# Performance work log

Measured on AMD Instinct MI355X. Metric: run time of the kernel, lower is better.

## Reference

```python
import jax, jax.numpy as jnp
import numpy as np
from jax import lax

SEQ_LEN, BC, NODES, FEAT, HID, NUM_LAYER = 12, 16, 1024, 32, 64, 2
NEG_BIG = -1e16


def _gru_layer(x_seq, w_ih, w_hh, b_ih, b_hh):
    # x_seq: [T, B, in]; PyTorch gate order r, z, n
    B = x_seq.shape[1]
    h0 = jnp.zeros((B, w_hh.shape[1]), dtype=x_seq.dtype)

    def step(h, x):
        gi = x @ w_ih.T + b_ih
        gh = h @ w_hh.T + b_hh
        ir, iz, inn = jnp.split(gi, 3, axis=-1)
        hr, hz, hn = jnp.split(gh, 3, axis=-1)
        r = jax.nn.sigmoid(ir + hr)
        zg = jax.nn.sigmoid(iz + hz)
        n = jnp.tanh(inn + r * hn)
        h_new = (1.0 - zg) * n + zg * h
        return h_new, h_new

    h_T, ys = lax.scan(step, h0, x_seq)
    return ys, h_T


def _gat_aggregate(z_, maskf):
    # z_: [bc, nodes, H]; inner-product attention with leaky_relu(0.1) and adjacency mask
    att = jnp.einsum('bnd,bmd->bnm', z_, z_)
    att = jax.nn.leaky_relu(att, negative_slope=0.1) * maskf[None]
    att = jnp.where(att == 0.0, NEG_BIG, att)  # masked_fill_(atten==0, -1e16)
    att = jax.nn.softmax(att, axis=2)
    return jnp.einsum('bnm,bmd->bnd', att, z_)


def setup_inputs() -> dict:
    key = jax.random.key(0)
    ks = jax.random.split(key, 12)
    s = 1.0 / np.sqrt(HID)
    inp = {
        'h': jax.random.normal(ks[0], (SEQ_LEN, BC, NODES, FEAT), dtype=jnp.float32),
        'mask': jax.random.randint(ks[1], (NODES, NODES), 0, 2, dtype=jnp.int32),
        'w_ih0': jax.random.uniform(ks[2], (3 * HID, FEAT), minval=-s, maxval=s),
        'w_hh0': jax.random.uniform(ks[3], (3 * HID, HID), minval=-s, maxval=s),
        'b_ih0': jax.random.uniform(ks[4], (3 * HID,), minval=-s, maxval=s),
        'b_hh0': jax.random.uniform(ks[5], (3 * HID,), minval=-s, maxval=s),
        'w_ih1': jax.random.uniform(ks[6], (3 * HID, HID), minval=-s, maxval=s),
        'w_hh1': jax.random.uniform(ks[7], (3 * HID, HID), minval=-s, maxval=s),
        'b_ih1': jax.random.uniform(ks[8], (3 * HID,), minval=-s, maxval=s),
        'b_hh1': jax.random.uniform(ks[9], (3 * HID,), minval=-s, maxval=s),
    }
    return inp


def reference(h, mask, w_ih0, w_hh0, b_ih0, b_hh0, w_ih1, w_hh1, b_ih1, b_hh1):
    x = h.reshape(SEQ_LEN, BC * NODES, FEAT)
    ys0, hT0 = _gru_layer(x, w_ih0, w_hh0, b_ih0, b_hh0)
    _, hT1 = _gru_layer(ys0, w_ih1, w_hh1, b_ih1, b_hh1)
    # z: [num_layer, bc, nodes, H]
    z = jnp.stack([hT0, hT1]).reshape(NUM_LAYER, BC, NODES, HID)
    maskf = mask.astype(z.dtype)
    h_agg = jax.vmap(_gat_aggregate, in_axes=(0, None))(z, maskf)
    return h_agg  # [num_layer, bc, nodes, H]
```

## Files before the change

### kernel.cpp

```cpp
#include <hip/hip_runtime.h>
#include <math.h>

#define SEQ 12
#define NBATCH 16384
#define FEAT 32
#define HID 64
#define NSPLIT 2

#define WP_IH0 0
#define WP_HH0 6144
#define WP_IH1 18432
#define WP_HH1 30720
#define WP_TOTAL 43008

typedef __attribute__((ext_vector_type(8))) short bf16x8;
typedef __attribute__((ext_vector_type(4))) float f32x4;

#define MFMA_B16(A,B,C) __builtin_amdgcn_mfma_f32_16x16x32_bf16((A),(B),(C),0,0,0)

union B8u { unsigned short s[8]; bf16x8 v; };

__device__ __forceinline__ float sigf(float x) { return 1.0f / (1.0f + __expf(-x)); }
__device__ __forceinline__ float tanh_fast(float x) { return 2.0f / (1.0f + __expf(-2.0f * x)) - 1.0f; }

__device__ __forceinline__ unsigned int packsplit(float v) {
  unsigned int u  = __float_as_uint(v);
  unsigned int hi = u & 0xFFFF0000u;
  unsigned int lo = __float_as_uint(v - __uint_as_float(hi)) >> 16;
  return hi | lo;
}

__device__ __forceinline__ void unpack8(const unsigned int* p, bf16x8& H, bf16x8& L) {
  uint4 u0 = *(const uint4*)p;
  uint4 u1 = *(const uint4*)(p + 4);
  unsigned int uu[8] = {u0.x, u0.y, u0.z, u0.w, u1.x, u1.y, u1.z, u1.w};
  B8u hh, ll;
  #pragma unroll
  for (int i = 0; i < 8; i++) {
    hh.s[i] = (unsigned short)(uu[i] >> 16);
    ll.s[i] = (unsigned short)(uu[i] & 0xFFFFu);
  }
  H = hh.v; L = ll.v;
}

__device__ __forceinline__ void split8(const float* fa, bf16x8& H, bf16x8& L) {
  B8u hh, ll;
  #pragma unroll
  for (int i = 0; i < 8; i++) {
    unsigned int u  = __float_as_uint(fa[i]);
    unsigned int hi = u & 0xFFFF0000u;
    hh.s[i] = (unsigned short)(hi >> 16);
    ll.s[i] = (unsigned short)(__float_as_uint(fa[i] - __uint_as_float(hi)) >> 16);
  }
  H = hh.v; L = ll.v;
}

#define DOT4(acc, A_, B_)                                   \
  acc = fmaf((A_).x, (B_).x, acc);                          \
  acc = fmaf((A_).y, (B_).y, acc);                          \
  acc = fmaf((A_).z, (B_).z, acc);                          \
  acc = fmaf((A_).w, (B_).w, acc);

__global__ void prep_frag_kernel(const float* __restrict__ w_ih0, const float* __restrict__ w_hh0,
                                 const float* __restrict__ w_ih1, const float* __restrict__ w_hh1,
                                 unsigned short* __restrict__ wf)
{
  int i = blockIdx.x * blockDim.x + threadIdx.x;
  if (i >= 43008) return;
  const float* src; int K, rel, baseS;
  if (i < 6144)       { src = w_ih0; K = 32; rel = i;         baseS = 0; }
  else if (i < 18432) { src = w_hh0; K = 64; rel = i - 6144;  baseS = 12288; }
  else if (i < 30720) { src = w_ih1; K = 64; rel = i - 18432; baseS = 36864; }
  else                { src = w_hh1; K = 64; rel = i - 30720; baseS = 61440; }
  int nks = K / 32;
  int fp   = rel >> 9;
  int lane = (rel >> 3) & 63;
  int e    = rel & 7;
  int ct = fp / nks, ks = fp % nks;
  int g = ct * 16 + (lane & 15);
  int k = ks * 32 + (lane >> 4) * 8 + e;
  float v = src[g * K + k];
  unsigned int u = __float_as_uint(v);
  unsigned short hi = (unsigned short)(u >> 16);
  float hif = __uint_as_float(u & 0xFFFF0000u);
  unsigned short lo = (unsigned short)(__float_as_uint(v - hif) >> 16);
  int out = baseS + fp * 1024 + lane * 8 + e;
  wf[out]       = hi;
  wf[out + 512] = lo;
}

__global__ void mask_pack(const int* __restrict__ mask, unsigned int* __restrict__ mbits)
{
  int i = blockIdx.x * blockDim.x + threadIdx.x;
  if (i >= 32768) return;
  int r = i >> 5, wd = i & 31;
  const int* mp = mask + (size_t)r * 1024 + wd * 32;
  unsigned int b = 0;
  #pragma unroll
  for (int k = 0; k < 32; k++) b |= (mp[k] != 0 ? 1u : 0u) << k;
  mbits[i] = b;
}

#define HSTR 72
__global__ __launch_bounds__(256, 2) void gru_fused(
    const float* __restrict__ x, const unsigned short* __restrict__ wf,
    const float* __restrict__ b_ih0, const float* __restrict__ b_hh0,
    const float* __restrict__ b_ih1, const float* __restrict__ b_hh1,
    unsigned int* __restrict__ zpk0, unsigned int* __restrict__ zpk1)
{
  __shared__ unsigned short h0h[2][16 * HSTR], h0o[2][16 * HSTR];
  __shared__ unsigned short h1h[2][16 * HSTR], h1o[2][16 * HSTR];
  const int tid = threadIdx.x;
  const int w = tid >> 6, l = tid & 63, lr = l & 15, lg = l >> 4;
  const int s0 = blockIdx.x * 16;
  const int j = w * 16 + lr;

  bf16x8 Wih0[3][2], Whh0[3][2][2], Wih1[3][2][2], Whh1[3][2][2];
  #pragma unroll
  for (int g = 0; g < 3; g++) {
    const int ct = w + g * 4;
    Wih0[g][0] = *(const bf16x8*)&wf[ct * 1024 + l * 8];
    Wih0[g][1] = *(const bf16x8*)&wf[ct * 1024 + 512 + l * 8];
    #pragma unroll
    for (int ks = 0; ks < 2; ks++) {
      Whh0[g][ks][0] = *(const bf16x8*)&wf[12288 + (ct * 2 + ks) * 1024 + l * 8];
      Whh0[g][ks][1] = *(const bf16x8*)&wf[12288 + (ct * 2 + ks) * 1024 + 512 + l * 8];
      Wih1[g][ks][0] = *(const bf16x8*)&wf[36864 + (ct * 2 + ks) * 1024 + l * 8];
      Wih1[g][ks][1] = *(const bf16x8*)&wf[36864 + (ct * 2 + ks) * 1024 + 512 + l * 8];
      Whh1[g][ks][0] = *(const bf16x8*)&wf[61440 + (ct * 2 + ks) * 1024 + l * 8];
      Whh1[g][ks][1] = *(const bf16x8*)&wf[61440 + (ct * 2 + ks) * 1024 + 512 + l * 8];
    }
  }

  const float br0  = b_ih0[j]      + b_hh0[j];
  const float bz0  = b_ih0[64 + j] + b_hh0[64 + j];
  const float bni0 = b_ih0[128 + j];
  const float bnh0 = b_hh0[128 + j];
  const float br1  = b_ih1[j]      + b_hh1[j];
  const float bz1  = b_ih1[64 + j] + b_hh1[64 + j];
  const float bni1 = b_ih1[128 + j];
  const float bnh1 = b_hh1[128 + j];

  for (int i = tid; i < 16 * HSTR; i += 256) {
    h0h[0][i] = 0; h0o[0][i] = 0; h1h[0][i] = 0; h1o[0][i] = 0;
  }
  float hD0[4] = {0.f, 0.f, 0.f, 0.f};
  float hD1[4] = {0.f, 0.f, 0.f, 0.f};
  __syncthreads();

  float4 xc0 = *(const float4*)(x + ((size_t)s0 + lr) * FEAT + lg * 8);
  float4 xc1 = *(const float4*)(x + ((size_t)s0 + lr) * FEAT + lg * 8 + 4);

  int pb = 0;
  #pragma unroll 1
  for (int t = 0; t < SEQ; t++) {
    const int cb = pb ^ 1;
    float4 xn0, xn1;
    if (t < SEQ - 1) {
      const float* xp = x + ((size_t)(t + 1) * NBATCH + s0 + lr) * FEAT + lg * 8;
      xn0 = *(const float4*)xp;
      xn1 = *(const float4*)(xp + 4);
    }

    f32x4 aR, aZ, aNI, aNH;
    #pragma unroll
    for (int e = 0; e < 4; e++) { aR[e] = br0; aZ[e] = bz0; aNI[e] = bni0; aNH[e] = bnh0; }
    {
      float fa[8] = {xc0.x, xc0.y, xc0.z, xc0.w, xc1.x, xc1.y, xc1.z, xc1.w};
      bf16x8 Ah, Al;
      split8(fa, Ah, Al);
      aR  = MFMA_B16(Ah, Wih0[0][0], aR);  aR  = MFMA_B16(Al, Wih0[0][0], aR);  aR  = MFMA_B16(Ah, Wih0[0][1], aR);
      aZ  = MFMA_B16(Ah, Wih0[1][0], aZ);  aZ  = MFMA_B16(Al, Wih0[1][0], aZ);  aZ  = MFMA_B16(Ah, Wih0[1][1], aZ);
      aNI = MFMA_B16(Ah, Wih0[2][0], aNI); aNI = MFMA_B16(Al, Wih0[2][0], aNI); aNI = MFMA_B16(Ah, Wih0[2][1], aNI);
    }
    #pragma unroll
    for (int ks = 0; ks < 2; ks++) {
      bf16x8 Ah = *(const bf16x8*)&h0h[pb][lr * HSTR + ks * 32 + lg * 8];
      bf16x8 Al = *(const bf16x8*)&h0o[pb][lr * HSTR + ks * 32 + lg * 8];
      aR  = MFMA_B16(Ah, Whh0[0][ks][0], aR);  aR  = MFMA_B16(Al, Whh0[0][ks][0], aR);  aR  = MFMA_B16(Ah, Whh0[0][ks][1], aR);
      aZ  = MFMA_B16(Ah, Whh0[1][ks][0], aZ);  aZ  = MFMA_B16(Al, Whh0[1][ks][0], aZ);  aZ  = MFMA_B16(Ah, Whh0[1][ks][1], aZ);
      aNH = MFMA_B16(Ah, Whh0[2][ks][0], aNH); aNH = MFMA_B16(Al, Whh0[2][ks][0], aNH); aNH = MFMA_B16(Ah, Whh0[2][ks][1], aNH);
    }
    #pragma unroll
    for (int e = 0; e < 4; e++) {
      float rg = sigf(aR[e]);
      float zg = sigf(aZ[e]);
      float n  = tanh_fast(fmaf(rg, aNH[e], aNI[e]));
      float hn = fmaf(zg, hD0[e] - n, n);
      hD0[e] = hn;
      unsigned int pk = packsplit(hn);
      int idx = (lg * 4 + e) * HSTR + j;
      h0h[cb][idx] = (unsigned short)(pk >> 16);
      h0o[cb][idx] = (unsigned short)(pk & 0xFFFFu);
    }
    __syncthreads();

    #pragma unroll
    for (int e = 0; e < 4; e++) { aR[e] = br1; aZ[e] = bz1; aNI[e] = bni1; aNH[e] = bnh1; }
    #pragma unroll
    for (int ks = 0; ks < 2; ks++) {
      bf16x8 Ah = *(const bf16x8*)&h0h[cb][lr * HSTR + ks * 32 + lg * 8];
      bf16x8 Al = *(const bf16x8*)&h0o[cb][lr * HSTR + ks * 32 + lg * 8];
      aR  = MFMA_B16(Ah, Wih1[0][ks][0], aR);  aR  = MFMA_B16(Al, Wih1[0][ks][0], aR);  aR  = MFMA_B16(Ah, Wih1[0][ks][1], aR);
      aZ  = MFMA_B16(Ah, Wih1[1][ks][0], aZ);  aZ  = MFMA_B16(Al, Wih1[1][ks][0], aZ);  aZ  = MFMA_B16(Ah, Wih1[1][ks][1], aZ);
      aNI = MFMA_B16(Ah, Wih1[2][ks][0], aNI); aNI = MFMA_B16(Al, Wih1[2][ks][0], aNI); aNI = MFMA_B16(Ah, Wih1[2][ks][1], aNI);
    }
    #pragma unroll
    for (int ks = 0; ks < 2; ks++) {
      bf16x8 Ah = *(const bf16x8*)&h1h[pb][lr * HSTR + ks * 32 + lg * 8];
      bf16x8 Al = *(const bf16x8*)&h1o[pb][lr * HSTR + ks * 32 + lg * 8];
      aR  = MFMA_B16(Ah, Whh1[0][ks][0], aR);  aR  = MFMA_B16(Al, Whh1[0][ks][0], aR);  aR  = MFMA_B16(Ah, Whh1[0][ks][1], aR);
      aZ  = MFMA_B16(Ah, Whh1[1][ks][0], aZ);  aZ  = MFMA_B16(Al, Whh1[1][ks][0], aZ);  aZ  = MFMA_B16(Ah, Whh1[1][ks][1], aZ);
      aNH = MFMA_B16(Ah, Whh1[2][ks][0], aNH); aNH = MFMA_B16(Al, Whh1[2][ks][0], aNH); aNH = MFMA_B16(Ah, Whh1[2][ks][1], aNH);
    }
    #pragma unroll
    for (int e = 0; e < 4; e++) {
      float rg = sigf(aR[e]);
      float zg = sigf(aZ[e]);
      float n  = tanh_fast(fmaf(rg, aNH[e], aNI[e]));
      float hn = fmaf(zg, hD1[e] - n, n);
      hD1[e] = hn;
      unsigned int pk = packsplit(hn);
      int idx = (lg * 4 + e) * HSTR + j;
      h1h[cb][idx] = (unsigned short)(pk >> 16);
      h1o[cb][idx] = (unsigned short)(pk & 0xFFFFu);
    }
    xc0 = xn0; xc1 = xn1;
    pb = cb;
  }

  #pragma unroll
  for (int e = 0; e < 4; e++) {
    int sl = lg * 4 + e;
    zpk0[(size_t)(s0 + sl) * 64 + j] = packsplit(hD0[e]);
    zpk1[(size_t)(s0 + sl) * 64 + j] = packsplit(hD1[e]);
  }
}

__global__ void prep_kernel(const float* __restrict__ w_ih0, const float* __restrict__ w_hh0,
                            const float* __restrict__ w_ih1, const float* __restrict__ w_hh1,
                            float* __restrict__ wp)
{
  for (int i = blockIdx.x * blockDim.x + threadIdx.x; i < WP_TOTAL; i += gridDim.x * blockDim.x) {
    const float* src;
    int K, rel;
    if (i < WP_HH0)      { src = w_ih0; K = 32; rel = i; }
    else if (i < WP_IH1) { src = w_hh0; K = 64; rel = i - WP_HH0; }
    else if (i < WP_HH1) { src = w_ih1; K = 64; rel = i - WP_IH1; }
    else                 { src = w_hh1; K = 64; rel = i - WP_HH1; }
    int kr = rel & 3;
    int jj = (rel >> 2) & 63;
    int rest = rel >> 8;
    int g = rest % 3;
    int k4 = rest / 3;
    wp[i] = src[(g * 64 + jj) * K + k4 * 4 + kr];
  }
}

__global__ __launch_bounds__(256, 1) void gru_fallback(
    const float* __restrict__ x, const float* __restrict__ wpack,
    const float* __restrict__ b_ih0, const float* __restrict__ b_hh0,
    const float* __restrict__ b_ih1, const float* __restrict__ b_hh1,
    unsigned int* __restrict__ zout)
{
  __shared__ float wlds[36864];
  __shared__ float h0s[16][64];
  __shared__ float h1s[16][64];
  const int tid = threadIdx.x;
  {
    const float4* src = (const float4*)(wpack + WP_HH0);
    float4* dst = (float4*)wlds;
    #pragma unroll 4
    for (int i = tid; i < 9216; i += 256) dst[i] = src[i];
  }
  const int j  = tid & 63;
  const int sg = __builtin_amdgcn_readfirstlane(tid >> 6);
  const float br0  = b_ih0[j]      + b_hh0[j];
  const float bz0  = b_ih0[64 + j] + b_hh0[64 + j];
  const float bni0 = b_ih0[128 + j];
  const float bnh0 = b_hh0[128 + j];
  const float br1  = b_ih1[j]      + b_hh1[j];
  const float bz1  = b_ih1[64 + j] + b_hh1[64 + j];
  const float bni1 = b_ih1[128 + j];
  const float bnh1 = b_hh1[128 + j];
  const int s0 = blockIdx.x * 16;
  float h0r[4] = {0.f, 0.f, 0.f, 0.f};
  float h1r[4] = {0.f, 0.f, 0.f, 0.f};
  #pragma unroll
  for (int ss = 0; ss < 4; ss++) { h0s[sg * 4 + ss][j] = 0.f; h1s[sg * 4 + ss][j] = 0.f; }
  __syncthreads();
  const float4* wih0g = (const float4*)(wpack + WP_IH0);
  const float4* whh0l = (const float4*)(wlds);
  const float4* wih1l = (const float4*)(wlds + 12288);
  const float4* whh1l = (const float4*)(wlds + 24576);
  for (int t = 0; t < SEQ; t++) {
    float ar[4], az[4], ani[4], anh[4];
    #pragma unroll
    for (int ss = 0; ss < 4; ss++) { ar[ss] = br0; az[ss] = bz0; ani[ss] = bni0; anh[ss] = bnh0; }
    const float4* xr0 = (const float4*)(x + ((size_t)t * NBATCH + (s0 + sg * 4 + 0)) * FEAT);
    const float4* xr1 = (const float4*)(x + ((size_t)t * NBATCH + (s0 + sg * 4 + 1)) * FEAT);
    const float4* xr2 = (const float4*)(x + ((size_t)t * NBATCH + (s0 + sg * 4 + 2)) * FEAT);
    const float4* xr3 = (const float4*)(x + ((size_t)t * NBATCH + (s0 + sg * 4 + 3)) * FEAT);
    #pragma unroll
    for (int k4 = 0; k4 < 8; k4++) {
      float4 wr = wih0g[(k4 * 3 + 0) * 64 + j];
      float4 wz = wih0g[(k4 * 3 + 1) * 64 + j];
      float4 wn = wih0g[(k4 * 3 + 2) * 64 + j];
      float4 xv[4] = {xr0[k4], xr1[k4], xr2[k4], xr3[k4]};
      #pragma unroll
      for (int ss = 0; ss < 4; ss++) {
        DOT4(ar[ss],  wr, xv[ss]);
        DOT4(az[ss],  wz, xv[ss]);
        DOT4(ani[ss], wn, xv[ss]);
      }
    }
    #pragma unroll
    for (int k4 = 0; k4 < 16; k4++) {
      float4 wr = whh0l[(k4 * 3 + 0) * 64 + j];
      float4 wz = whh0l[(k4 * 3 + 1) * 64 + j];
      float4 wn = whh0l[(k4 * 3 + 2) * 64 + j];
      #pragma unroll
      for (int ss = 0; ss < 4; ss++) {
        float4 hv = *(const float4*)&h0s[sg * 4 + ss][k4 * 4];
        DOT4(ar[ss],  wr, hv);
        DOT4(az[ss],  wz, hv);
        DOT4(anh[ss], wn, hv);
      }
    }
    float h0n[4];
    #pragma unroll
    for (int ss = 0; ss < 4; ss++) {
      float rg = sigf(ar[ss]);
      float zg = sigf(az[ss]);
      float ng = tanh_fast(fmaf(rg, anh[ss], ani[ss]));
      h0n[ss] = fmaf(zg, h0r[ss] - ng, ng);
    }
    __syncthreads();
    #pragma unroll
    for (int ss = 0; ss < 4; ss++) { h0s[sg * 4 + ss][j] = h0n[ss]; h0r[ss] = h0n[ss]; }
    __syncthreads();
    #pragma unroll
    for (int ss = 0; ss < 4; ss++) { ar[ss] = br1; az[ss] = bz1; ani[ss] = bni1; anh[ss] = bnh1; }
    #pragma unroll
    for (int k4 = 0; k4 < 16; k4++) {
      float4 wr = wih1l[(k4 * 3 + 0) * 64 + j];
      float4 wz = wih1l[(k4 * 3 + 1) * 64 + j];
      float4 wn = wih1l[(k4 * 3 + 2) * 64 + j];
      #pragma unroll
      for (int ss = 0; ss < 4; ss++) {
        float4 hv = *(const float4*)&h0s[sg * 4 + ss][k4 * 4];
        DOT4(ar[ss],  wr, hv);
        DOT4(az[ss],  wz, hv);
        DOT4(ani[ss], wn, hv);
      }
    }
    #pragma unroll
    for (int k4 = 0; k4 < 16; k4++) {
      float4 wr = whh1l[(k4 * 3 + 0) * 64 + j];
      float4 wz = whh1l[(k4 * 3 + 1) * 64 + j];
      float4 wn = whh1l[(k4 * 3 + 2) * 64 + j];
      #pragma unroll
      for (int ss = 0; ss < 4; ss++) {
        float4 hv = *(const float4*)&h1s[sg * 4 + ss][k4 * 4];
        DOT4(ar[ss],  wr, hv);
        DOT4(az[ss],  wz, hv);
        DOT4(anh[ss], wn, hv);
      }
    }
    float h1n[4];
    #pragma unroll
    for (int ss = 0; ss < 4; ss++) {
      float rg = sigf(ar[ss]);
      float zg = sigf(az[ss]);
      float ng = tanh_fast(fmaf(rg, anh[ss], ani[ss]));
      h1n[ss] = fmaf(zg, h1r[ss] - ng, ng);
    }
    __syncthreads();
    #pragma unroll
    for (int ss = 0; ss < 4; ss++) { h1s[sg * 4 + ss][j] = h1n[ss]; h1r[ss] = h1n[ss]; }
    __syncthreads();
  }
  #pragma unroll
  for (int ss = 0; ss < 4; ss++) {
    int s = s0 + sg * 4 + ss;
    zout[(size_t)s * 64 + j]            = packsplit(h0r[ss]);
    zout[(size_t)(NBATCH + s) * 64 + j] = packsplit(h1r[ss]);
  }
}

__global__ __launch_bounds__(256, 4) void gat_mfma4(
    const unsigned int* __restrict__ zpk, const unsigned int* __restrict__ mbits,
    float* __restrict__ partO, float* __restrict__ partD,
    float* __restrict__ out, int nsplit)
{
  __shared__ unsigned int VT[64 * 68];
  __shared__ float        PS[64 * 68];
  const int tid = threadIdx.x;
  const int w = tid >> 6, l = tid & 63, lr = l & 15, lg = l >> 4;
  const int blk  = blockIdx.x;
  const int lbrt = blk / nsplit;
  const int half = blk - lbrt * nsplit;
  const int rt = lbrt & 15;
  const int lb = lbrt >> 4;
  const int tiles = 16 / nsplit;
  const int mt0 = half * tiles;
  const unsigned int* zb = zpk + (size_t)lb * 65536;
  const int n0 = rt * 64;

  bf16x8 Qh[2], Ql[2];
  #pragma unroll
  for (int ks = 0; ks < 2; ks++)
    unpack8(&zb[(size_t)(n0 + w * 16 + lr) * 64 + ks * 32 + lg * 8], Qh[ks], Ql[ks]);

  unsigned int vpre[16];
  #pragma unroll
  for (int r = 0; r < 16; r++)
    vpre[r] = zb[(size_t)(mt0 * 64 + w * 16 + r) * 64 + l];

  f32x4 O[4];
  float D[4] = {0.f, 0.f, 0.f, 0.f};
  #pragma unroll
  for (int ct = 0; ct < 4; ct++)
    #pragma unroll
    for (int e = 0; e < 4; e++) O[ct][e] = 0.f;

  #pragma unroll 1
  for (int mt = mt0; mt < mt0 + tiles; ++mt) {
    __syncthreads();
    #pragma unroll
    for (int q = 0; q < 4; q++)
      *(uint4*)&VT[l * 68 + w * 16 + q * 4] =
          make_uint4(vpre[q * 4], vpre[q * 4 + 1], vpre[q * 4 + 2], vpre[q * 4 + 3]);
    {
      const int nt = (mt + 1 < mt0 + tiles) ? (mt + 1) : mt0;
      #pragma unroll
      for (int r = 0; r < 16; r++)
        vpre[r] = zb[(size_t)(nt * 64 + w * 16 + r) * 64 + l];
    }
    __syncthreads();

    f32x4 S[4];
    #pragma unroll
    for (int ct = 0; ct < 4; ct++)
      #pragma unroll
      for (int e = 0; e < 4; e++) S[ct][e] = 0.f;
    #pragma unroll
    for (int ks = 0; ks < 2; ks++) {
      #pragma unroll
      for (int ct = 0; ct < 4; ct++) {
        bf16x8 Kh, Kl;
        unpack8(&zb[(size_t)(mt * 64 + ct * 16 + lr) * 64 + ks * 32 + lg * 8], Kh, Kl);
        S[ct] = MFMA_B16(Qh[ks], Kh, S[ct]);
        S[ct] = MFMA_B16(Ql[ks], Kh, S[ct]);
        S[ct] = MFMA_B16(Qh[ks], Kl, S[ct]);
      }
    }

    #pragma unroll
    for (int e = 0; e < 4; e++) {
      const int row = n0 + w * 16 + lg * 4 + e;
      const uint2 mw = *(const uint2*)&mbits[(size_t)row * 32 + mt * 2];
      const unsigned int sel[4] = {mw.x >> lr, mw.x >> (16 + lr), mw.y >> lr, mw.y >> (16 + lr)};
      float ds = 0.f;
      #pragma unroll
      for (int ct = 0; ct < 4; ct++) {
        float v = S[ct][e];
        float lrv = v > 0.f ? v : 0.1f * v;
        float p = ((sel[ct] & 1u) && lrv != 0.0f) ? __expf(lrv - 64.0f) : 0.0f;
        ds += p;
        PS[(w * 16 + lg * 4 + e) * 68 + ct * 16 + lr] = p;
      }
      D[e] += ds;
    }

    #pragma unroll
    for (int ks = 0; ks < 2; ks++) {
      const float* pp = &PS[(w * 16 + lr) * 68 + ks * 32 + lg * 8];
      float4 p0 = *(const float4*)pp;
      float4 p1 = *(const float4*)(pp + 4);
      float fa[8] = {p0.x, p0.y, p0.z, p0.w, p1.x, p1.y, p1.z, p1.w};
      B8u H;
      #pragma unroll
      for (int i = 0; i < 8; i++)
        H.s[i] = (unsigned short)((__float_as_uint(fa[i]) + 0x8000u) >> 16);
      bf16x8 Ph = H.v;
      #pragma unroll
      for (int ct = 0; ct < 4; ct++) {
        bf16x8 Vh, Vl;
        unpack8(&VT[(ct * 16 + lr) * 68 + ks * 32 + lg * 8], Vh, Vl);
        O[ct] = MFMA_B16(Ph, Vh, O[ct]);
        O[ct] = MFMA_B16(Ph, Vl, O[ct]);
      }
    }
  }

  #pragma unroll
  for (int e = 0; e < 4; e++) {
    #pragma unroll
    for (int sw = 1; sw < 16; sw <<= 1) D[e] += __shfl_xor(D[e], sw, 16);
  }

  if (nsplit == 1) {
    #pragma unroll
    for (int e = 0; e < 4; e++) {
      float inv = 1.0f / D[e];
      size_t rowo = ((size_t)lb * 1024 + n0 + w * 16 + lg * 4 + e) * 64;
      #pragma unroll
      for (int ct = 0; ct < 4; ct++)
        out[rowo + ct * 16 + lr] = O[ct][e] * inv;
    }
  } else {
    float* po = partO + (size_t)blk * 4096;
    #pragma unroll
    for (int e = 0; e < 4; e++) {
      int row = w * 16 + lg * 4 + e;
      #pragma unroll
      for (int ct = 0; ct < 4; ct++)
        po[row * 64 + ct * 16 + lr] = O[ct][e];
      if (lr == 0) partD[(size_t)blk * 64 + row] = D[e];
    }
  }
}

__global__ __launch_bounds__(256) void gat_combine(
    const float* __restrict__ partO, const float* __restrict__ partD,
    float* __restrict__ out, int nsplit)
{
  const int lbrt = blockIdx.x;
  const int q  = threadIdx.x >> 2;
  const int dc = (threadIdx.x & 3) * 16;
  float dt = 0.f;
  for (int i = 0; i < nsplit; i++) dt += partD[(size_t)(lbrt * nsplit + i) * 64 + q];
  float inv = 1.0f / dt;
  float* op = out + ((size_t)lbrt * 64 + q) * 64 + dc;
  #pragma unroll
  for (int v = 0; v < 4; v++) {
    float4 acc = make_float4(0.f, 0.f, 0.f, 0.f);
    for (int i = 0; i < nsplit; i++) {
      const float4 o = *(const float4*)(partO + (size_t)(lbrt * nsplit + i) * 4096 + q * 64 + dc + v * 4);
      acc.x += o.x; acc.y += o.y; acc.z += o.z; acc.w += o.w;
    }
    *(float4*)(op + v * 4) = make_float4(acc.x * inv, acc.y * inv, acc.z * inv, acc.w * inv);
  }
}

extern "C" void kernel_launch(void* const* d_in, const int* in_sizes, int n_in,
                              void* d_out, int out_size, void* d_ws, size_t ws_size,
                              hipStream_t stream) {
  const float* h     = (const float*)d_in[0];
  const int*   mask  = (const int*)d_in[1];
  const float* w_ih0 = (const float*)d_in[2];
  const float* w_hh0 = (const float*)d_in[3];
  const float* b_ih0 = (const float*)d_in[4];
  const float* b_hh0 = (const float*)d_in[5];
  const float* w_ih1 = (const float*)d_in[6];
  const float* w_hh1 = (const float*)d_in[7];
  const float* b_ih1 = (const float*)d_in[8];
  const float* b_hh1 = (const float*)d_in[9];
  float* out = (float*)d_out;

  char* wsb = (char*)d_ws;
  unsigned int* zpk = (unsigned int*)wsb;
  const size_t Z_BYTES  = (size_t)2 * NBATCH * 64 * 4;
  const size_t PART_OFF = Z_BYTES + 176128;
  const size_t PO_BYTES = (size_t)512 * NSPLIT * 4096 * 4;
  const size_t PD_BYTES = (size_t)512 * NSPLIT * 64 * 4;
  const size_t MB_OFF   = PART_OFF + PO_BYTES + PD_BYTES;
  const size_t NEED_FAST = MB_OFF + 131072;

  if (ws_size >= NEED_FAST) {
    unsigned short* wfrag = (unsigned short*)(wsb + Z_BYTES);
    float* partO  = (float*)(wsb + PART_OFF);
    float* partD  = (float*)(wsb + PART_OFF + PO_BYTES);
    unsigned int* mbits = (unsigned int*)(wsb + MB_OFF);
    prep_frag_kernel<<<168, 256, 0, stream>>>(w_ih0, w_hh0, w_ih1, w_hh1, wfrag);
    mask_pack<<<128, 256, 0, stream>>>(mask, mbits);
    gru_fused<<<1024, 256, 0, stream>>>(h, wfrag, b_ih0, b_hh0, b_ih1, b_hh1,
                                        zpk, zpk + (size_t)NBATCH * 64);
    gat_mfma4<<<512 * NSPLIT, 256, 0, stream>>>(zpk, mbits, partO, partD, out, NSPLIT);
    gat_combine<<<512, 256, 0, stream>>>(partO, partD, out, NSPLIT);
  } else {
    float* wpack = (float*)(wsb + Z_BYTES);
    unsigned int* mbits = (unsigned int*)(wsb + Z_BYTES + 172032);
    prep_kernel<<<24, 256, 0, stream>>>(w_ih0, w_hh0, w_ih1, w_hh1, wpack);
    mask_pack<<<128, 256, 0, stream>>>(mask, mbits);
    gru_fallback<<<1024, 256, 0, stream>>>(h, wpack, b_ih0, b_hh0, b_ih1, b_hh1, zpk);
    gat_mfma4<<<512, 256, 0, stream>>>(zpk, mbits, nullptr, nullptr, out, 1);
  }
}
```

Baseline: 167.6 us.

## Skew GRU layers across timesteps to share one barrier per step

Layer 0 step t+1 now runs in the same iteration as layer 1 step t. Both read the same layer-0 hidden state from shared memory, which removes one __syncthreads per timestep and lets the two layers' MFMA chains interleave. The first layer-0 step is peeled into a prologue that drops the zero-state matmul, and x is prefetched two steps ahead. The cost is more live accumulator registers and extra buffer-index bookkeeping.

```diff
diff --git a/kernel.cpp b/kernel.cpp
--- a/kernel.cpp
+++ b/kernel.cpp
@@ -141,92 +141,120 @@
   const float bni1 = b_ih1[128 + j];
   const float bnh1 = b_hh1[128 + j];
 
-  for (int i = tid; i < 16 * HSTR; i += 256) {
-    h0h[0][i] = 0; h0o[0][i] = 0; h1h[0][i] = 0; h1o[0][i] = 0;
-  }
+  for (int i = tid; i < 16 * HSTR; i += 256) { h1h[1][i] = 0; h1o[1][i] = 0; }
   float hD0[4] = {0.f, 0.f, 0.f, 0.f};
   float hD1[4] = {0.f, 0.f, 0.f, 0.f};
+
+  {
+    f32x4 aR, aZ, aNI;
+    #pragma unroll
+    for (int e = 0; e < 4; e++) { aR[e] = br0; aZ[e] = bz0; aNI[e] = bni0; }
+    const float* xp = x + ((size_t)s0 + lr) * FEAT + lg * 8;
+    float4 a0 = *(const float4*)xp;
+    float4 a1 = *(const float4*)(xp + 4);
+    float fa[8] = {a0.x, a0.y, a0.z, a0.w, a1.x, a1.y, a1.z, a1.w};
+    bf16x8 Ah, Al;
+    split8(fa, Ah, Al);
+    aR  = MFMA_B16(Ah, Wih0[0][0], aR);  aR  = MFMA_B16(Al, Wih0[0][0], aR);  aR  = MFMA_B16(Ah, Wih0[0][1], aR);
+    aZ  = MFMA_B16(Ah, Wih0[1][0], aZ);  aZ  = MFMA_B16(Al, Wih0[1][0], aZ);  aZ  = MFMA_B16(Ah, Wih0[1][1], aZ);
+    aNI = MFMA_B16(Ah, Wih0[2][0], aNI); aNI = MFMA_B16(Al, Wih0[2][0], aNI); aNI = MFMA_B16(Ah, Wih0[2][1], aNI);
+    #pragma unroll
+    for (int e = 0; e < 4; e++) {
+      float rg = sigf(aR[e]);
+      float zg = sigf(aZ[e]);
+      float n  = tanh_fast(fmaf(rg, bnh0, aNI[e]));
+      float hn = (1.0f - zg) * n;
+      hD0[e] = hn;
+      unsigned int pk = packsplit(hn);
+      int idx = (lg * 4 + e) * HSTR + j;
+      h0h[0][idx] = (unsigned short)(pk >> 16);
+      h0o[0][idx] = (unsigned short)(pk & 0xFFFFu);
+    }
+  }
   __syncthreads();
 
-  float4 xc0 = *(const float4*)(x + ((size_t)s0 + lr) * FEAT + lg * 8);
-  float4 xc1 = *(const float4*)(x + ((size_t)s0 + lr) * FEAT + lg * 8 + 4);
-
-  int pb = 0;
+  float4 xc0 = *(const float4*)(x + ((size_t)NBATCH + s0 + lr) * FEAT + lg * 8);
+  float4 xc1 = *(const float4*)(x + ((size_t)NBATCH + s0 + lr) * FEAT + lg * 8 + 4);
+
   #pragma unroll 1
   for (int t = 0; t < SEQ; t++) {
-    const int cb = pb ^ 1;
+    const int rd = t & 1;
+    const int wr = rd ^ 1;
     float4 xn0, xn1;
-    if (t < SEQ - 1) {
-      const float* xp = x + ((size_t)(t + 1) * NBATCH + s0 + lr) * FEAT + lg * 8;
+    if (t < SEQ - 2) {
+      const float* xp = x + ((size_t)(t + 2) * NBATCH + s0 + lr) * FEAT + lg * 8;
       xn0 = *(const float4*)xp;
       xn1 = *(const float4*)(xp + 4);
     }
 
-    f32x4 aR, aZ, aNI, aNH;
-    #pragma unroll
-    for (int e = 0; e < 4; e++) { aR[e] = br0; aZ[e] = bz0; aNI[e] = bni0; aNH[e] = bnh0; }
-    {
+    f32x4 aR1, aZ1, aNI1, aNH1;
+    f32x4 aR0, aZ0, aNI0, aNH0;
+    #pragma unroll
+    for (int e = 0; e < 4; e++) {
+      aR1[e] = br1; aZ1[e] = bz1; aNI1[e] = bni1; aNH1[e] = bnh1;
+      aR0[e] = br0; aZ0[e] = bz0; aNI0[e] = bni0; aNH0[e] = bnh0;
+    }
+
+    const bool doL0 = (t < SEQ - 1);
+    if (doL0) {
       float fa[8] = {xc0.x, xc0.y, xc0.z, xc0.w, xc1.x, xc1.y, xc1.z, xc1.w};
       bf16x8 Ah, Al;
       split8(fa, Ah, Al);
-      aR  = MFMA_B16(Ah, Wih0[0][0], aR);  aR  = MFMA_B16(Al, Wih0[0][0], aR);  aR  = MFMA_B16(Ah, Wih0[0][1], aR);
-      aZ  = MFMA_B16(Ah, Wih0[1][0], aZ);  aZ  = MFMA_B16(Al, Wih0[1][0], aZ);  aZ  = MFMA_B16(Ah, Wih0[1][1], aZ);
-      aNI = MFMA_B16(Ah, Wih0[2][0], aNI); aNI = MFMA_B16(Al, Wih0[2][0], aNI); aNI = MFMA_B16(Ah, Wih0[2][1], aNI);
-    }
+      aR0  = MFMA_B16(Ah, Wih0[0][0], aR0);  aR0  = MFMA_B16(Al, Wih0[0][0], aR0);  aR0  = MFMA_B16(Ah, Wih0[0][1], aR0);
+      aZ0  = MFMA_B16(Ah, Wih0[1][0], aZ0);  aZ0  = MFMA_B16(Al, Wih0[1][0], aZ0);  aZ0  = MFMA_B16(Ah, Wih0[1][1], aZ0);
+      aNI0 = MFMA_B16(Ah, Wih0[2][0], aNI0); aNI0 = MFMA_B16(Al, Wih0[2][0], aNI0); aNI0 = MFMA_B16(Ah, Wih0[2][1], aNI0);
+    }
+
     #pragma unroll
     for (int ks = 0; ks < 2; ks++) {
-      bf16x8 Ah = *(const bf16x8*)&h0h[pb][lr * HSTR + ks * 32 + lg * 8];
-      bf16x8 Al = *(const bf16x8*)&h0o[pb][lr * HSTR + ks * 32 + lg * 8];
-      aR  = MFMA_B16(Ah, Whh0[0][ks][0], aR);  aR  = MFMA_B16(Al, Whh0[0][ks][0], aR);  aR  = MFMA_B16(Ah, Whh0[0][ks][1], aR);
-      aZ  = MFMA_B16(Ah, Whh0[1][ks][0], aZ);  aZ  = MFMA_B16(Al, Whh0[1][ks][0], aZ);  aZ  = MFMA_B16(Ah, Whh0[1][ks][1], aZ);
-      aNH = MFMA_B16(Ah, Whh0[2][ks][0], aNH); aNH = MFMA_B16(Al, Whh0[2][ks][0], aNH); aNH = MFMA_B16(Ah, Whh0[2][ks][1], aNH);
-    }
+      bf16x8 Ah = *(const bf16x8*)&h0h[rd][lr * HSTR + ks * 32 + lg * 8];
+      bf16x8 Al = *(const bf16x8*)&h0o[rd][lr * HSTR + ks * 32 + lg * 8];
+      aR1  = MFMA_B16(Ah, Wih1[0][ks][0], aR1);  aR1  = MFMA_B16(Al, Wih1[0][ks][0], aR1);  aR1  = MFMA_B16(Ah, Wih1[0][ks][1], aR1);
+      aZ1  = MFMA_B16(Ah, Wih1[1][ks][0], aZ1);  aZ1  = MFMA_B16(Al, Wih1[1][ks][0], aZ1);  aZ1  = MFMA_B16(Ah, Wih1[1][ks][1], aZ1);
+      aNI1 = MFMA_B16(Ah, Wih1[2][ks][0], aNI1); aNI1 = MFMA_B16(Al, Wih1[2][ks][0], aNI1); aNI1 = MFMA_B16(Ah, Wih1[2][ks][1], aNI1);
+      if (doL0) {
+        aR0  = MFMA_B16(Ah, Whh0[0][ks][0], aR0);  aR0  = MFMA_B16(Al, Whh0[0][ks][0], aR0);  aR0  = MFMA_B16(Ah, Whh0[0][ks][1], aR0);
+        aZ0  = MFMA_B16(Ah, Whh0[1][ks][0], aZ0);  aZ0  = MFMA_B16(Al, Whh0[1][ks][0], aZ0);  aZ0  = MFMA_B16(Ah, Whh0[1][ks][1], aZ0);
+        aNH0 = MFMA_B16(Ah, Whh0[2][ks][0], aNH0); aNH0 = MFMA_B16(Al, Whh0[2][ks][0], aNH0); aNH0 = MFMA_B16(Ah, Whh0[2][ks][1], aNH0);
+      }
+    }
+    #pragma unroll
+    for (int ks = 0; ks < 2; ks++) {
+      bf16x8 Ah = *(const bf16x8*)&h1h[rd ^ 1][lr * HSTR + ks * 32 + lg * 8];
+      bf16x8 Al = *(const bf16x8*)&h1o[rd ^ 1][lr * HSTR + ks * 32 + lg * 8];
+      aR1  = MFMA_B16(Ah, Whh1[0][ks][0], aR1);  aR1  = MFMA_B16(Al, Whh1[0][ks][0], aR1);  aR1  = MFMA_B16(Ah, Whh1[0][ks][1], aR1);
+      aZ1  = MFMA_B16(Ah, Whh1[1][ks][0], aZ1);  aZ1  = MFMA_B16(Al, Whh1[1][ks][0], aZ1);  aZ1  = MFMA_B16(Ah, Whh1[1][ks][1], aZ1);
+      aNH1 = MFMA_B16(Ah, Whh1[2][ks][0], aNH1); aNH1 = MFMA_B16(Al, Whh1[2][ks][0], aNH1); aNH1 = MFMA_B16(Ah, Whh1[2][ks][1], aNH1);
+    }
+
     #pragma unroll
     for (int e = 0; e < 4; e++) {
-      float rg = sigf(aR[e]);
-      float zg = sigf(aZ[e]);
-      float n  = tanh_fast(fmaf(rg, aNH[e], aNI[e]));
-      float hn = fmaf(zg, hD0[e] - n, n);
-      hD0[e] = hn;
-      unsigned int pk = packsplit(hn);
-      int idx = (lg * 4 + e) * HSTR + j;
-      h0h[cb][idx] = (unsigned short)(pk >> 16);
-      h0o[cb][idx] = (unsigned short)(pk & 0xFFFFu);
-    }
-    __syncthreads();
-
-    #pragma unroll
-    for (int e = 0; e < 4; e++) { aR[e] = br1; aZ[e] = bz1; aNI[e] = bni1; aNH[e] = bnh1; }
-    #pragma unroll
-    for (int ks = 0; ks < 2; ks++) {
-      bf16x8 Ah = *(const bf16x8*)&h0h[cb][lr * HSTR + ks * 32 + lg * 8];
-      bf16x8 Al = *(const bf16x8*)&h0o[cb][lr * HSTR + ks * 32 + lg * 8];
-      aR  = MFMA_B16(Ah, Wih1[0][ks][0], aR);  aR  = MFMA_B16(Al, Wih1[0][ks][0], aR);  aR  = MFMA_B16(Ah, Wih1[0][ks][1], aR);
-      aZ  = MFMA_B16(Ah, Wih1[1][ks][0], aZ);  aZ  = MFMA_B16(Al, Wih1[1][ks][0], aZ);  aZ  = MFMA_B16(Ah, Wih1[1][ks][1], aZ);
-      aNI = MFMA_B16(Ah, Wih1[2][ks][0], aNI); aNI = MFMA_B16(Al, Wih1[2][ks][0], aNI); aNI = MFMA_B16(Ah, Wih1[2][ks][1], aNI);
-    }
-    #pragma unroll
-    for (int ks = 0; ks < 2; ks++) {
-      bf16x8 Ah = *(const bf16x8*)&h1h[pb][lr * HSTR + ks * 32 + lg * 8];
-      bf16x8 Al = *(const bf16x8*)&h1o[pb][lr * HSTR + ks * 32 + lg * 8];
-      aR  = MFMA_B16(Ah, Whh1[0][ks][0], aR);  aR  = MFMA_B16(Al, Whh1[0][ks][0], aR);  aR  = MFMA_B16(Ah, Whh1[0][ks][1], aR);
-      aZ  = MFMA_B16(Ah, Whh1[1][ks][0], aZ);  aZ  = MFMA_B16(Al, Whh1[1][ks][0], aZ);  aZ  = MFMA_B16(Ah, Whh1[1][ks][1], aZ);
-      aNH = MFMA_B16(Ah, Whh1[2][ks][0], aNH); aNH = MFMA_B16(Al, Whh1[2][ks][0], aNH); aNH = MFMA_B16(Ah, Whh1[2][ks][1], aNH);
-    }
-    #pragma unroll
-    for (int e = 0; e < 4; e++) {
-      float rg = sigf(aR[e]);
-      float zg = sigf(aZ[e]);
-      float n  = tanh_fast(fmaf(rg, aNH[e], aNI[e]));
+      float rg = sigf(aR1[e]);
+      float zg = sigf(aZ1[e]);
+      float n  = tanh_fast(fmaf(rg, aNH1[e], aNI1[e]));
       float hn = fmaf(zg, hD1[e] - n, n);
       hD1[e] = hn;
       unsigned int pk = packsplit(hn);
       int idx = (lg * 4 + e) * HSTR + j;
-      h1h[cb][idx] = (unsigned short)(pk >> 16);
-      h1o[cb][idx] = (unsigned short)(pk & 0xFFFFu);
-    }
+      h1h[rd][idx] = (unsigned short)(pk >> 16);
+      h1o[rd][idx] = (unsigned short)(pk & 0xFFFFu);
+    }
+    if (doL0) {
+      #pragma unroll
+      for (int e = 0; e < 4; e++) {
+        float rg = sigf(aR0[e]);
+        float zg = sigf(aZ0[e]);
+        float n  = tanh_fast(fmaf(rg, aNH0[e], aNI0[e]));
+        float hn = fmaf(zg, hD0[e] - n, n);
+        hD0[e] = hn;
+        unsigned int pk = packsplit(hn);
+        int idx = (lg * 4 + e) * HSTR + j;
+        h0h[wr][idx] = (unsigned short)(pk >> 16);
+        h0o[wr][idx] = (unsigned short)(pk & 0xFFFFu);
+      }
+    }
+    __syncthreads();
     xc0 = xn0; xc1 = xn1;
-    pb = cb;
   }
 
   #pragma unroll
```

After: 173.2 us. +3.3%, slower.
